# Kernel optimization log

Hardware: AMD Instinct MI355X
Metric: run time of the kernel (lower is better)

Reference implementation:

```python
import jax, jax.numpy as jnp
import numpy as np

NUM_FRAMES = 8
HEAD_DIM = 32


def setup_inputs() -> dict:
    key = jax.random.key(0)
    k1, k2, k3, k4, k5 = jax.random.split(key, 5)
    dim = 384
    nh = dim // HEAD_DIM
    return {
        "x": jax.random.normal(k1, (16, dim, 16, 16), dtype=jnp.float32),
        "qk_w": jax.random.normal(k2, (2 * dim, dim), dtype=jnp.float32) * 0.02,
        "alpha": jax.random.normal(k3, (1, nh, 1, 1), dtype=jnp.float32),
        "beta": jax.random.normal(k4, (1, nh, 1, 1), dtype=jnp.float32),
        "gamma": jax.random.normal(k5, (1, nh, 1, 1), dtype=jnp.float32),
    }


def reference(x, qk_w, alpha, beta, gamma):
    B_T, C, H, W = x.shape
    B = B_T // NUM_FRAMES
    N = NUM_FRAMES * H * W
    nh = C // HEAD_DIM
    scale = HEAD_DIM ** -0.5

    # [B*T,C,H,W] -> [B,N,C] tokens (frames-major token order, matching torch)
    xt = x.reshape(B, NUM_FRAMES, C, H, W).transpose(0, 2, 1, 3, 4)  # B,C,T,H,W
    xt = xt.reshape(B, C, N).transpose(0, 2, 1)                      # B,N,C

    qk = (xt @ qk_w.T).reshape(B, N, 2, nh, HEAD_DIM)
    qk = qk.transpose(2, 0, 3, 1, 4)                                 # 2,B,nh,N,hd
    q, k = qk[0], qk[1]
    v = xt.reshape(B, N, nh, HEAD_DIM).transpose(0, 2, 1, 3)         # B,nh,N,hd

    attn = jax.nn.softmax(jnp.einsum('bhnd,bhmd->bhnm', q * scale, k), axis=-1)
    eye = jnp.eye(N, dtype=x.dtype)
    Cm = jnp.full((N, N), 1.0 / N, dtype=x.dtype)
    attn = alpha * eye + beta * attn - gamma * Cm                    # B,nh,N,N

    out = jnp.einsum('bhnm,bhmd->bhnd', attn, v)
    out = out.transpose(0, 2, 1, 3).reshape(B, N, C)                 # B,N,C
    out = out.transpose(0, 2, 1).reshape(B, C, NUM_FRAMES, H, W)
    out = out.transpose(0, 2, 1, 3, 4).reshape(B_T, C, H, W)
    return out
```

## Files before the change

kernel.cpp:

```cpp
#include <hip/hip_runtime.h>
#include <hip/hip_bf16.h>

typedef __attribute__((ext_vector_type(8))) short short8;
typedef __attribute__((ext_vector_type(2))) float f32x2;
typedef __attribute__((ext_vector_type(16))) float f32x16;
typedef __attribute__((ext_vector_type(4))) unsigned int uint4v;
typedef unsigned short ushort_t;
typedef unsigned int uint_t;

#define NFRAMES 8
#define HD 32
#define CDIM 384
#define NH 12
#define NTOK 2048
#define QKCOLS 768
#define TILEB 2048
#define QSCALE 0.2550541213313367f

static __device__ __forceinline__ ushort_t f2bf(float f) {
    __hip_bfloat16 h = __float2bfloat16(f);
    return *reinterpret_cast<ushort_t*>(&h);
}
static __device__ __forceinline__ uint_t packbf2(float lo, float hi) {
    return (uint_t)f2bf(lo) | ((uint_t)f2bf(hi) << 16);
}

__global__ __launch_bounds__(256) void pack_kernel(const float* __restrict__ x,
                                                   const float* __restrict__ qk_w,
                                                   ushort_t* __restrict__ Xt,
                                                   ushort_t* __restrict__ VFG,
                                                   float* __restrict__ psum,
                                                   ushort_t* __restrict__ Wb) {
    int tid = threadIdx.x;
    int bid = blockIdx.x;
    if (bid >= 192) {
        int vid = (bid - 192) * 256 + tid;
        int j = vid / 48;
        float scale = (j < CDIM) ? QSCALE : 1.0f;
        const float* src = qk_w + vid * 8;
        float4 a = *(const float4*)src;
        float4 b = *(const float4*)(src + 4);
        uint4 o = make_uint4(packbf2(a.x * scale, a.y * scale), packbf2(a.z * scale, a.w * scale),
                             packbf2(b.x * scale, b.y * scale), packbf2(b.z * scale, b.w * scale));
        *(uint4*)(Wb + vid * 8) = o;
        return;
    }
    __shared__ float lds[32 * 257];
    __shared__ float red[8][32];
    int bt = bid & 15;
    int h = bid >> 4;
    int c0 = h * 32;
    const float* src = x + ((long)bt * CDIM + c0) * 256;
#pragma unroll
    for (int i = 0; i < 32; ++i) lds[i * 257 + tid] = src[i * 256 + tid];
    __syncthreads();
    int b = bt >> 3, t = bt & 7;
    long n = (long)b * NTOK + t * 256 + tid;
    uint4* dst = reinterpret_cast<uint4*>(Xt + n * CDIM + c0);
#pragma unroll
    for (int k = 0; k < 4; ++k) {
        uint_t vv[4];
#pragma unroll
        for (int q = 0; q < 4; ++q)
            vv[q] = packbf2(lds[(k * 8 + q * 2) * 257 + tid], lds[(k * 8 + q * 2 + 1) * 257 + tid]);
        dst[k] = make_uint4(vv[0], vv[1], vv[2], vv[3]);
    }
    int bh = b * NH + h;
#pragma unroll
    for (int pass = 0; pass < 4; ++pass) {
        int kt = pass * 2 + (tid >> 7);
        int slot = tid & 127;
        int d = slot & 31, c2 = slot >> 5;
        const float* p0 = &lds[d * 257 + kt * 32 + c2 * 8];
        uint4 o = make_uint4(packbf2(p0[0], p0[1]), packbf2(p0[2], p0[3]),
                             packbf2(p0[4], p0[5]), packbf2(p0[6], p0[7]));
        *(uint4*)((char*)VFG + ((size_t)(bh * 64 + t * 8 + kt)) * TILEB + slot * 16) = o;
    }
    int ch = tid & 31, seg = tid >> 5;
    float s = 0.f;
#pragma unroll
    for (int j = 0; j < 32; ++j) s += lds[ch * 257 + seg * 32 + j];
    red[seg][ch] = s;
    __syncthreads();
    if (tid < 32) {
        float tot = 0.f;
#pragma unroll
        for (int i = 0; i < 8; ++i) tot += red[i][tid];
        psum[(bt * NH + h) * HD + tid] = tot;
    }
}

__global__ __launch_bounds__(256) void proj_kernel(const ushort_t* __restrict__ Xt,
                                                   const ushort_t* __restrict__ Wb,
                                                   ushort_t* __restrict__ QFG,
                                                   ushort_t* __restrict__ KFG) {
    __shared__ __align__(16) ushort_t tb[4][32][40];
    int tid = threadIdx.x;
    int lane = tid & 63;
    int w = tid >> 6;
    int wid = blockIdx.x * 4 + w;
    int mb = wid / 24, nb = wid % 24;
    int j31 = lane & 31, hi = lane >> 5;
    const char* Arow = (const char*)(Xt + (mb * 32 + j31) * CDIM + hi * 8);
    const char* Brow = (const char*)(Wb + (nb * 32 + j31) * CDIM + hi * 8);
    f32x16 acc = {};
#pragma unroll
    for (int k16 = 0; k16 < 24; ++k16) {
        short8 a = *(const short8*)(Arow + k16 * 32);
        short8 bb = *(const short8*)(Brow + k16 * 32);
        acc = __builtin_amdgcn_mfma_f32_32x32x16_bf16(a, bb, acc, 0, 0, 0);
    }
#pragma unroll
    for (int q = 0; q < 16; ++q) {
        int row = (q & 3) + 8 * (q >> 2) + 4 * hi;
        tb[w][row][j31] = f2bf(acc[q]);
    }
    short8 f0 = *(const short8*)&tb[w][j31][hi * 8];
    short8 f1 = *(const short8*)&tb[w][j31][16 + hi * 8];
    int bsel = mb >> 6;
    int tile = mb & 63;
    int hh = (nb < 12) ? nb : nb - 12;
    ushort_t* dstbuf = (nb < 12) ? QFG : KFG;
    char* base = (char*)dstbuf + ((size_t)((bsel * NH + hh) * 64 + tile)) * TILEB;
    *(short8*)(base + lane * 16) = f0;
    *(short8*)(base + 1024 + lane * 16) = f1;
}

__global__ __launch_bounds__(512) void attn_kernel(
    const ushort_t* __restrict__ QFG, const ushort_t* __restrict__ KFG,
    const ushort_t* __restrict__ VFG, const float* __restrict__ x,
    const float* __restrict__ psum, const float* __restrict__ alpha,
    const float* __restrict__ beta, const float* __restrict__ gamma,
    float* __restrict__ out) {
    __shared__ float mrg[4 * 1088 + 32];

    int tid = threadIdx.x, lane = tid & 63, w = tid >> 6;
    int bid = blockIdx.x;
    int L = (bid & 7) * 192 + (bid >> 3);
    int qc = L & 63, bh = L >> 6;
    int h = bh % NH, b = bh / NH;
    int j31 = lane & 31, hi = lane >> 5;
    int qb = qc * 32;

    const char* Qb = (const char*)QFG + ((size_t)(bh * 64 + qc)) * TILEB + lane * 16;
    short8 qf0 = *(const short8*)(Qb);
    short8 qf1 = *(const short8*)(Qb + 1024);

    const char* Kbase = (const char*)KFG + ((size_t)(bh * 64 + w * 8)) * TILEB + lane * 16;
    const char* Vbase = (const char*)VFG + ((size_t)(bh * 64 + w * 8)) * TILEB + lane * 16;

    f32x16 acc = {};
    f32x2 lp2 = {};

#pragma unroll
    for (int i = 0; i < 8; ++i) {
        size_t off = (size_t)i * TILEB;
        short8 K0 = *(const short8*)(Kbase + off);
        short8 K1 = *(const short8*)(Kbase + off + 1024);
        short8 V0 = *(const short8*)(Vbase + off);
        short8 V1 = *(const short8*)(Vbase + off + 1024);
        f32x16 s = {};
        __builtin_amdgcn_s_setprio(1);
        s = __builtin_amdgcn_mfma_f32_32x32x16_bf16(K0, qf0, s, 0, 0, 0);
        s = __builtin_amdgcn_mfma_f32_32x32x16_bf16(K1, qf1, s, 0, 0, 0);
        __builtin_amdgcn_s_setprio(0);
        uint_t pk[8];
#pragma unroll
        for (int j = 0; j < 8; ++j) {
            float e0 = __builtin_amdgcn_exp2f(s[2 * j]);
            float e1 = __builtin_amdgcn_exp2f(s[2 * j + 1]);
            f32x2 ee;
            ee[0] = e0;
            ee[1] = e1;
            lp2 += ee;
            asm("v_cvt_pk_bf16_f32 %0, %1, %2" : "=v"(pk[j]) : "v"(e0), "v"(e1));
        }
#pragma unroll
        for (int kh = 0; kh < 2; ++kh) {
            uint_t o0 = pk[kh * 4], o1 = pk[kh * 4 + 1];
            uint_t o2 = pk[kh * 4 + 2], o3 = pk[kh * 4 + 3];
            auto r02 = __builtin_amdgcn_permlane32_swap(o2, o0, false, false);
            auto r13 = __builtin_amdgcn_permlane32_swap(o3, o1, false, false);
            uint4v uu;
            uu[0] = r02[1];
            uu[1] = r13[1];
            uu[2] = r02[0];
            uu[3] = r13[0];
            short8 pa = __builtin_bit_cast(short8, uu);
            __builtin_amdgcn_s_setprio(1);
            acc = __builtin_amdgcn_mfma_f32_32x32x16_bf16(pa, (kh ? V1 : V0), acc, 0, 0, 0);
            __builtin_amdgcn_s_setprio(0);
        }
    }

    float lp = lp2[0] + lp2[1];

    float* reg = mrg + (w & 3) * 1088;
    if (w < 4) {
#pragma unroll
        for (int q = 0; q < 16; ++q) reg[lane * 17 + q] = acc[q];
        reg[lane * 17 + 16] = lp;
    }
    __syncthreads();
    if (w >= 4) {
#pragma unroll
        for (int q = 0; q < 16; ++q) reg[lane * 17 + q] += acc[q];
        reg[lane * 17 + 16] += lp;
    }
    __syncthreads();
    if (w < 2) {
        float* rb = mrg + (w + 2) * 1088;
#pragma unroll
        for (int q = 0; q < 16; ++q) reg[lane * 17 + q] += rb[lane * 17 + q];
        reg[lane * 17 + 16] += rb[lane * 17 + 16];
    }
    __syncthreads();
    if (w == 0) {
#pragma unroll
        for (int q = 0; q < 16; ++q) acc[q] = mrg[lane * 17 + q] + mrg[1088 + lane * 17 + q];
        float lsum = mrg[lane * 17 + 16] + mrg[1088 + lane * 17 + 16];
        lsum += __shfl_xor(lsum, 32);
        float* Lb = mrg + 4 * 1088;
        if (!hi) Lb[j31] = lsum;
        float alpha_h = alpha[h], beta_h = beta[h], gamma_h = gamma[h];
        int d = j31, c = h * HD + d;
        float sv = 0.f;
#pragma unroll
        for (int t = 0; t < NFRAMES; ++t) sv += psum[((b * NFRAMES + t) * NH + h) * HD + d];
        float gsv = gamma_h * sv * (1.0f / NTOK);
#pragma unroll
        for (int q = 0; q < 16; ++q) {
            int qrow = (q & 3) + 8 * (q >> 2) + 4 * hi;
            int n = qb + qrow;
            float linv = 1.0f / Lb[qrow];
            long xidx = ((long)(b * NFRAMES + (n >> 8)) * CDIM + c) * 256 + (n & 255);
            out[xidx] = beta_h * acc[q] * linv + alpha_h * x[xidx] - gsv;
        }
    }
}

extern "C" void kernel_launch(void* const* d_in, const int* in_sizes, int n_in,
                              void* d_out, int out_size, void* d_ws, size_t ws_size,
                              hipStream_t stream) {
    const float* x = (const float*)d_in[0];
    const float* qk_w = (const float*)d_in[1];
    const float* alpha = (const float*)d_in[2];
    const float* beta = (const float*)d_in[3];
    const float* gamma = (const float*)d_in[4];
    float* out = (float*)d_out;

    char* ws = (char*)d_ws;
    ushort_t* Xt = (ushort_t*)ws;
    ushort_t* Wb = (ushort_t*)(ws + 3145728);
    ushort_t* QFG = (ushort_t*)(ws + 3735552);
    ushort_t* KFG = (ushort_t*)(ws + 6881280);
    ushort_t* VFG = (ushort_t*)(ws + 10027008);
    float* psum = (float*)(ws + 13172736);

    hipLaunchKernelGGL(pack_kernel, dim3(336), dim3(256), 0, stream, x, qk_w, Xt, VFG, psum, Wb);
    hipLaunchKernelGGL(proj_kernel, dim3(768), dim3(256), 0, stream, Xt, Wb, QFG, KFG);
    hipLaunchKernelGGL(attn_kernel, dim3(1536), dim3(512), 0, stream,
                       QFG, KFG, VFG, x, psum, alpha, beta, gamma, out);
}
```

Before: 54.29 us.

## Register-block projection GEMM 2x2 per wave and use packbf2 in attention

Each wave in the projection kernel now computes a 64x64 output block with four MFMA accumulators instead of one 32x32 tile. This reuses each loaded A and B fragment twice and cuts global operand loads per output. The launch drops to 384 blocks of 128 threads, which lowers parallelism and raises register pressure. In the attention kernel, the inline-asm packed bf16 conversion is replaced by the software packbf2 helper. That may add instructions in the hot loop, since it likely rounds each value separately instead of using one packed convert.

```diff
diff --git a/kernel.cpp b/kernel.cpp
--- a/kernel.cpp
+++ b/kernel.cpp
@@ -90,40 +90,56 @@
     }
 }
 
-__global__ __launch_bounds__(256) void proj_kernel(const ushort_t* __restrict__ Xt,
+__global__ __launch_bounds__(128) void proj_kernel(const ushort_t* __restrict__ Xt,
                                                    const ushort_t* __restrict__ Wb,
                                                    ushort_t* __restrict__ QFG,
                                                    ushort_t* __restrict__ KFG) {
-    __shared__ __align__(16) ushort_t tb[4][32][40];
+    __shared__ __align__(16) ushort_t tb[2][32][40];
     int tid = threadIdx.x;
     int lane = tid & 63;
     int w = tid >> 6;
-    int wid = blockIdx.x * 4 + w;
-    int mb = wid / 24, nb = wid % 24;
+    int wid = blockIdx.x * 2 + w;
+    int mb2 = wid / 12, nb2 = wid % 12;
     int j31 = lane & 31, hi = lane >> 5;
-    const char* Arow = (const char*)(Xt + (mb * 32 + j31) * CDIM + hi * 8);
-    const char* Brow = (const char*)(Wb + (nb * 32 + j31) * CDIM + hi * 8);
-    f32x16 acc = {};
+    const char* A0 = (const char*)(Xt + (mb2 * 64 + j31) * CDIM + hi * 8);
+    const char* A1 = A0 + 32 * CDIM * 2;
+    const char* B0 = (const char*)(Wb + (nb2 * 64 + j31) * CDIM + hi * 8);
+    const char* B1 = B0 + 32 * CDIM * 2;
+    f32x16 acc00 = {}, acc01 = {}, acc10 = {}, acc11 = {};
 #pragma unroll
     for (int k16 = 0; k16 < 24; ++k16) {
-        short8 a = *(const short8*)(Arow + k16 * 32);
-        short8 bb = *(const short8*)(Brow + k16 * 32);
-        acc = __builtin_amdgcn_mfma_f32_32x32x16_bf16(a, bb, acc, 0, 0, 0);
-    }
-#pragma unroll
-    for (int q = 0; q < 16; ++q) {
-        int row = (q & 3) + 8 * (q >> 2) + 4 * hi;
-        tb[w][row][j31] = f2bf(acc[q]);
-    }
-    short8 f0 = *(const short8*)&tb[w][j31][hi * 8];
-    short8 f1 = *(const short8*)&tb[w][j31][16 + hi * 8];
-    int bsel = mb >> 6;
-    int tile = mb & 63;
-    int hh = (nb < 12) ? nb : nb - 12;
-    ushort_t* dstbuf = (nb < 12) ? QFG : KFG;
-    char* base = (char*)dstbuf + ((size_t)((bsel * NH + hh) * 64 + tile)) * TILEB;
-    *(short8*)(base + lane * 16) = f0;
-    *(short8*)(base + 1024 + lane * 16) = f1;
+        short8 a0 = *(const short8*)(A0 + k16 * 32);
+        short8 a1 = *(const short8*)(A1 + k16 * 32);
+        short8 b0 = *(const short8*)(B0 + k16 * 32);
+        short8 b1 = *(const short8*)(B1 + k16 * 32);
+        acc00 = __builtin_amdgcn_mfma_f32_32x32x16_bf16(a0, b0, acc00, 0, 0, 0);
+        acc01 = __builtin_amdgcn_mfma_f32_32x32x16_bf16(a0, b1, acc01, 0, 0, 0);
+        acc10 = __builtin_amdgcn_mfma_f32_32x32x16_bf16(a1, b0, acc10, 0, 0, 0);
+        acc11 = __builtin_amdgcn_mfma_f32_32x32x16_bf16(a1, b1, acc11, 0, 0, 0);
+    }
+#pragma unroll
+    for (int rr = 0; rr < 2; ++rr) {
+#pragma unroll
+        for (int cc = 0; cc < 2; ++cc) {
+            const f32x16& acc = rr ? (cc ? acc11 : acc10) : (cc ? acc01 : acc00);
+#pragma unroll
+            for (int q = 0; q < 16; ++q) {
+                int row = (q & 3) + 8 * (q >> 2) + 4 * hi;
+                tb[w][row][j31] = f2bf(acc[q]);
+            }
+            short8 f0 = *(const short8*)&tb[w][j31][hi * 8];
+            short8 f1 = *(const short8*)&tb[w][j31][16 + hi * 8];
+            int mtile = mb2 * 2 + rr;
+            int bsel = mtile >> 6;
+            int tile = mtile & 63;
+            int hcol = nb2 * 2 + cc;
+            int hh = (hcol < 12) ? hcol : hcol - 12;
+            ushort_t* dstbuf = (hcol < 12) ? QFG : KFG;
+            char* base = (char*)dstbuf + ((size_t)((bsel * NH + hh) * 64 + tile)) * TILEB;
+            *(short8*)(base + lane * 16) = f0;
+            *(short8*)(base + 1024 + lane * 16) = f1;
+        }
+    }
 }
 
 __global__ __launch_bounds__(512) void attn_kernel(
@@ -173,7 +189,7 @@
             ee[0] = e0;
             ee[1] = e1;
             lp2 += ee;
-            asm("v_cvt_pk_bf16_f32 %0, %1, %2" : "=v"(pk[j]) : "v"(e0), "v"(e1));
+            pk[j] = packbf2(e0, e1);
         }
 #pragma unroll
         for (int kh = 0; kh < 2; ++kh) {
@@ -258,7 +274,7 @@
     float* psum = (float*)(ws + 13172736);
 
     hipLaunchKernelGGL(pack_kernel, dim3(336), dim3(256), 0, stream, x, qk_w, Xt, VFG, psum, Wb);
-    hipLaunchKernelGGL(proj_kernel, dim3(768), dim3(256), 0, stream, Xt, Wb, QFG, KFG);
+    hipLaunchKernelGGL(proj_kernel, dim3(384), dim3(128), 0, stream, Xt, Wb, QFG, KFG);
     hipLaunchKernelGGL(attn_kernel, dim3(1536), dim3(512), 0, stream,
                        QFG, KFG, VFG, x, psum, alpha, beta, gamma, out);
 }
```

Result: faster. 52.36 us (-3.6%).
